# Kernel optimization log

Measured on AMD Instinct MI355X. Metric: run time of the kernel, lower is better.

The kernel has to match this reference:

```python
import jax, jax.numpy as jnp
import numpy as np

N = 10000        # num_nodes
E = 160000       # num_edges (before self loops)
D_IN = 256       # input_dim
H = 128          # hidden_dim (= per-head out_channels)
HEADS = 4
HD = HEADS * H   # 512
L = 16           # num_layers
OUT = 1024       # output_dim
G = 8            # num graphs in batch
EPS = 1e-5


def _layer_norm(x, w, b):
    m = jnp.mean(x, axis=-1, keepdims=True)
    v = jnp.mean(jnp.square(x - m), axis=-1, keepdims=True)
    return (x - m) / jnp.sqrt(v + EPS) * w + b


def setup_inputs() -> dict:
    key = jax.random.key(0)
    ks = jax.random.split(key, 20)
    s = 0.05
    x = jax.random.normal(ks[0], (N, D_IN), jnp.float32)
    edge_index = jax.random.randint(ks[1], (2, E), 0, N, dtype=jnp.int64)
    batch = jnp.sort(jax.random.randint(ks[2], (N,), 0, G, dtype=jnp.int64))
    return {
        "x": x,
        "edge_index": edge_index,
        "batch": batch,
        "W_in": jax.random.normal(ks[3], (D_IN, H), jnp.float32) * s,
        "b_in": jnp.zeros((H,), jnp.float32),
        "ln_in_w": jnp.ones((H,), jnp.float32),
        "ln_in_b": jnp.zeros((H,), jnp.float32),
        "Wsrc": jax.random.normal(ks[4], (L, H, HD), jnp.float32) * s,
        "Wdst": jax.random.normal(ks[5], (L, H, HD), jnp.float32) * s,
        "att_src": jax.random.normal(ks[6], (L, HEADS, H), jnp.float32) * s,
        "att_dst": jax.random.normal(ks[7], (L, HEADS, H), jnp.float32) * s,
        "Wout": jax.random.normal(ks[8], (L, HD, H), jnp.float32) * s,
        "bout": jnp.zeros((L, H), jnp.float32),
        "ln_w": jnp.ones((L, H), jnp.float32),
        "ln_b": jnp.zeros((L, H), jnp.float32),
        "Wp1": jax.random.normal(ks[9], (H, OUT), jnp.float32) * s,
        "bp1": jnp.zeros((OUT,), jnp.float32),
        "Wp2": jax.random.normal(ks[10], (OUT, OUT), jnp.float32) * s,
        "bp2": jnp.zeros((OUT,), jnp.float32),
    }


def reference(x, edge_index, batch, W_in, b_in, ln_in_w, ln_in_b,
              Wsrc, Wdst, att_src, att_dst, Wout, bout, ln_w, ln_b,
              Wp1, bp1, Wp2, bp2):
    # add self loops once (same edge set every layer)
    loop = jnp.arange(N, dtype=edge_index.dtype)
    e_src = jnp.concatenate([edge_index[0], loop])  # x_j (source)
    e_dst = jnp.concatenate([edge_index[1], loop])  # x_i (target / aggregate index)

    h = jax.nn.relu(_layer_norm(x @ W_in + b_in, ln_in_w, ln_in_b))  # [N, H]

    for l in range(L):
        hs = (h[e_src] @ Wsrc[l]).reshape(-1, HEADS, H)  # [E2, heads, H]
        hd = (h[e_dst] @ Wdst[l]).reshape(-1, HEADS, H)
        a = jnp.sum(hs * att_src[l], axis=-1) + jnp.sum(hd * att_dst[l], axis=-1)  # [E2, heads]
        a = jax.nn.leaky_relu(a, 0.2)
        # NOTE: faithful to source -- softmax over HEADS per edge, not over neighbors
        a = jax.nn.softmax(a, axis=-1)
        msg = (hs * a[..., None]).reshape(-1, HD)  # [E2, HD]
        agg = jax.ops.segment_sum(msg, e_dst, num_segments=N)  # [N, HD]
        out = agg @ Wout[l] + bout[l]
        h = jax.nn.relu(_layer_norm(out + h, ln_w[l], ln_b[l]))  # residual: H == H

    g = jax.ops.segment_max(h, batch, num_segments=G)  # global max pool [G, H]
    g = jax.nn.relu(g @ Wp1 + bp1)
    return g @ Wp2 + bp2  # [G, OUT]
```

## Files before the change

### kernel.cpp

```cpp
#include <hip/hip_runtime.h>
#include <hip/hip_bf16.h>

#define N_NODES 10000
#define E_EDGES 160000
#define E2 (E_EDGES + N_NODES)
#define D_IN 256
#define H 128
#define HEADS 4
#define HD 512
#define L_LAYERS 16
#define OUT_DIM 1024
#define G_GRAPHS 8
#define EPS 1e-5f
#define SPAD 10016

typedef unsigned short ushort_t;
typedef __attribute__((ext_vector_type(8))) short short8;
typedef __attribute__((ext_vector_type(4))) float f32x4;
typedef __attribute__((ext_vector_type(4))) unsigned u32x4;

__device__ __forceinline__ f32x4 mfma16(short8 a, short8 b, f32x4 c) {
    return __builtin_amdgcn_mfma_f32_16x16x32_bf16(a, b, c, 0, 0, 0);
}
__device__ __forceinline__ unsigned short f2b(float f) {
    unsigned u = __float_as_uint(f);
    u += 0x7fffu + ((u >> 16) & 1u);
    return (unsigned short)(u >> 16);
}
__device__ __forceinline__ float b2f(unsigned short b) {
    return __uint_as_float((unsigned)b << 16);
}
__device__ __forceinline__ unsigned pk2(float lo, float hi) {
    __hip_bfloat162 p = __float22bfloat162_rn(make_float2(lo, hi));
    return *(unsigned*)&p;
}

__global__ void k_zero(int* deg, int* cur, unsigned* g) {
    int i = blockIdx.x * blockDim.x + threadIdx.x;
    if (i < N_NODES) { deg[i] = 0; cur[i] = 0; }
    if (i < G_GRAPHS * H) g[i] = 0u;
}

__global__ void k_count(const int* ei, int* deg) {
    int e = blockIdx.x * blockDim.x + threadIdx.x;
    if (e >= E2) return;
    int d = (e < E_EDGES) ? ei[E_EDGES + e] : (e - E_EDGES);
    atomicAdd(&deg[d], 1);
}

__global__ void k_scan(const int* deg, int* rs) {
    __shared__ int s[1024];
    int t = threadIdx.x;
    int base = t * 10;
    int loc[10], run = 0;
    #pragma unroll
    for (int i = 0; i < 10; i++) {
        int idx = base + i;
        int v = (idx < N_NODES) ? deg[idx] : 0;
        loc[i] = run; run += v;
    }
    s[t] = run;
    __syncthreads();
    for (int off = 1; off < 1024; off <<= 1) {
        int xv = (t >= off) ? s[t - off] : 0;
        __syncthreads();
        s[t] += xv;
        __syncthreads();
    }
    int excl = s[t] - run;
    #pragma unroll
    for (int i = 0; i < 10; i++) {
        int idx = base + i;
        if (idx <= N_NODES) rs[idx] = excl + loc[i];
    }
}

__global__ void k_fill(const int* ei, const int* rs, int* cur, int* elist) {
    int e = blockIdx.x * blockDim.x + threadIdx.x;
    if (e >= E2) return;
    int s, d;
    if (e < E_EDGES) { s = ei[e]; d = ei[E_EDGES + e]; }
    else { s = d = e - E_EDGES; }
    int pos = atomicAdd(&cur[d], 1);
    elist[rs[d] + pos] = s;
}

__global__ __launch_bounds__(256) void k_vw(const float* __restrict__ Wsrc,
        const float* __restrict__ Wdst, const float* __restrict__ att_src,
        const float* __restrict__ att_dst, float* __restrict__ vsrc,
        float* __restrict__ vdst) {
    int t = threadIdx.x, w = t >> 6, lane = t & 63;
    int unit = blockIdx.x * 4 + w;
    int j = unit & 127, head = (unit >> 7) & 3, l = unit >> 9;
    int k2 = lane * 2;
    const float2 ws = *(const float2*)(Wsrc + (size_t)l * H * HD + (size_t)j * HD + head * 128 + k2);
    const float2 wd = *(const float2*)(Wdst + (size_t)l * H * HD + (size_t)j * HD + head * 128 + k2);
    const float2 as = *(const float2*)(att_src + (size_t)l * HEADS * H + head * 128 + k2);
    const float2 ad = *(const float2*)(att_dst + (size_t)l * HEADS * H + head * 128 + k2);
    float p = ws.x * as.x + ws.y * as.y;
    float q = wd.x * ad.x + wd.y * ad.y;
    #pragma unroll
    for (int off = 32; off > 0; off >>= 1) {
        p += __shfl_down(p, off);
        q += __shfl_down(q, off);
    }
    if (lane == 0) {
        vsrc[(size_t)l * HD + head * H + j] = p;
        vdst[(size_t)l * HD + head * H + j] = q;
    }
}

__global__ __launch_bounds__(256) void k_mm(const float* __restrict__ Wsrc,
        const float* __restrict__ Wout, float* __restrict__ M) {
    __shared__ float As[32][33];
    __shared__ float Bs[32][128];
    int bid = blockIdx.x;
    int q = bid & 3, hh = (bid >> 2) & 3, l = bid >> 4;
    int t = threadIdx.x;
    int ty = t >> 4, tx = t & 15;
    const float* WsB = Wsrc + (size_t)l * H * HD + (size_t)hh * 128;
    const float* WoB = Wout + (size_t)l * HD * H + (size_t)hh * 128 * H;
    float acc[2][8];
    #pragma unroll
    for (int r = 0; r < 2; r++)
        #pragma unroll
        for (int c = 0; c < 8; c++) acc[r][c] = 0.f;
    for (int kt = 0; kt < 4; kt++) {
        #pragma unroll
        for (int i = 0; i < 4; i++) {
            int lin = i * 256 + t;
            int rr = lin >> 5, cc = lin & 31;
            As[rr][cc] = WsB[(size_t)(q * 32 + rr) * HD + kt * 32 + cc];
        }
        #pragma unroll
        for (int i = 0; i < 16; i++) {
            int lin = i * 256 + t;
            int rr = lin >> 7, cc = lin & 127;
            Bs[rr][cc] = WoB[(size_t)(kt * 32 + rr) * H + cc];
        }
        __syncthreads();
        #pragma unroll
        for (int kk = 0; kk < 32; kk++) {
            float a0 = As[ty * 2][kk], a1 = As[ty * 2 + 1][kk];
            float4 b0 = *(const float4*)&Bs[kk][tx * 8];
            float4 b1 = *(const float4*)&Bs[kk][tx * 8 + 4];
            acc[0][0] += a0 * b0.x; acc[0][1] += a0 * b0.y;
            acc[0][2] += a0 * b0.z; acc[0][3] += a0 * b0.w;
            acc[0][4] += a0 * b1.x; acc[0][5] += a0 * b1.y;
            acc[0][6] += a0 * b1.z; acc[0][7] += a0 * b1.w;
            acc[1][0] += a1 * b0.x; acc[1][1] += a1 * b0.y;
            acc[1][2] += a1 * b0.z; acc[1][3] += a1 * b0.w;
            acc[1][4] += a1 * b1.x; acc[1][5] += a1 * b1.y;
            acc[1][6] += a1 * b1.z; acc[1][7] += a1 * b1.w;
        }
        __syncthreads();
    }
    #pragma unroll
    for (int r = 0; r < 2; r++)
        #pragma unroll
        for (int c = 0; c < 8; c++)
            M[(size_t)l * HD * H + (size_t)(hh * 128 + q * 32 + ty * 2 + r) * H + tx * 8 + c]
                = acc[r][c];
}

__global__ void k_pack_out2(const float* M, ushort_t* Wh, ushort_t* Wl) {
    int idx = blockIdx.x * 256 + threadIdx.x;
    int l = idx >> 16, rem = idx & 65535;
    int k = rem >> 7, col = rem & 127;
    float v = M[(size_t)l * HD * H + (size_t)k * H + col];
    unsigned short hi = f2b(v);
    unsigned short lo = f2b(v - b2f(hi));
    int nt = col >> 4, ks = k >> 5, lhi = (k >> 3) & 3, llo = col & 15, j = k & 7;
    size_t addr = (size_t)l * 65536 + (((size_t)(nt * 16 + ks) * 64) + lhi * 16 + llo) * 8 + j;
    Wh[addr] = hi;
    Wl[addr] = lo;
}

__global__ void k_pack_win(const float* W, ushort_t* Wp) {
    int idx = blockIdx.x * 256 + threadIdx.x;
    int k = idx >> 7, col = idx & 127;
    float v = W[(size_t)k * H + col];
    int nt = col >> 4, ks = k >> 5, lhi = (k >> 3) & 3, llo = col & 15, j = k & 7;
    Wp[(((size_t)(nt * 8 + ks) * 64) + lhi * 16 + llo) * 8 + j] = f2b(v);
}

__global__ __launch_bounds__(256) void k_in_mfma(
        const float* __restrict__ x, const ushort_t* __restrict__ WpI,
        const float* __restrict__ b_in, const float* __restrict__ lnw,
        const float* __restrict__ lnb, const float* __restrict__ vs,
        const float* __restrict__ vd, float* __restrict__ as0, float* __restrict__ ad0,
        float* __restrict__ h, ushort_t* __restrict__ hb) {
    __shared__ float part1[4][16], part2[4][16];
    __shared__ float apart[4][8][16];
    int t = threadIdx.x, w = t >> 6, lane = t & 63;
    int row0 = blockIdx.x * 16;
    int ar = lane & 15, ac = (lane >> 4) * 8;
    short8 a[8];
    #pragma unroll
    for (int ks = 0; ks < 8; ks++) {
        const float* xp = x + (size_t)(row0 + ar) * D_IN + ks * 32 + ac;
        float4 xa = *(const float4*)xp;
        float4 xb = *(const float4*)(xp + 4);
        u32x4 u;
        u.x = pk2(xa.x, xa.y); u.y = pk2(xa.z, xa.w);
        u.z = pk2(xb.x, xb.y); u.w = pk2(xb.z, xb.w);
        a[ks] = *(short8*)&u;
    }
    const ushort_t* B0 = WpI + ((size_t)(w * 2 + 0) * 8) * 64 * 8;
    const ushort_t* B1 = WpI + ((size_t)(w * 2 + 1) * 8) * 64 * 8;
    f32x4 c0 = {0.f, 0.f, 0.f, 0.f}, c1 = {0.f, 0.f, 0.f, 0.f};
    #pragma unroll
    for (int ks = 0; ks < 8; ks++) {
        short8 b0 = *(const short8*)(B0 + ((size_t)ks * 64 + lane) * 8);
        short8 b1 = *(const short8*)(B1 + ((size_t)ks * 64 + lane) * 8);
        c0 = mfma16(a[ks], b0, c0);
        c1 = mfma16(a[ks], b1, c1);
    }
    int col0 = w * 32 + ar, col1 = w * 32 + 16 + ar;
    int rb = (lane >> 4) * 4;
    float v0[4], v1[4], y0[4], y1[4];
    #pragma unroll
    for (int r = 0; r < 4; r++) {
        v0[r] = c0[r] + b_in[col0];
        v1[r] = c1[r] + b_in[col1];
        float p1 = v0[r] + v1[r];
        float p2 = v0[r] * v0[r] + v1[r] * v1[r];
        #pragma unroll
        for (int off = 1; off < 16; off <<= 1) {
            p1 += __shfl_xor(p1, off);
            p2 += __shfl_xor(p2, off);
        }
        if (ar == 0) { part1[w][rb + r] = p1; part2[w][rb + r] = p2; }
    }
    __syncthreads();
    #pragma unroll
    for (int r = 0; r < 4; r++) {
        int lr = rb + r;
        int row = row0 + lr;
        float s1 = part1[0][lr] + part1[1][lr] + part1[2][lr] + part1[3][lr];
        float s2 = part2[0][lr] + part2[1][lr] + part2[2][lr] + part2[3][lr];
        float m = s1 * (1.f / 128.f);
        float var = s2 * (1.f / 128.f) - m * m;
        float is = rsqrtf(var + EPS);
        y0[r] = fmaxf((v0[r] - m) * is * lnw[col0] + lnb[col0], 0.f);
        y1[r] = fmaxf((v1[r] - m) * is * lnw[col1] + lnb[col1], 0.f);
        h[(size_t)row * H + col0] = y0[r];
        h[(size_t)row * H + col1] = y1[r];
        hb[(size_t)row * H + col0] = f2b(y0[r]);
        hb[(size_t)row * H + col1] = f2b(y1[r]);
    }
    #pragma unroll
    for (int comp = 0; comp < 8; comp++) {
        float vc0 = (comp < 4) ? vs[comp * H + col0] : vd[(comp - 4) * H + col0];
        float vc1 = (comp < 4) ? vs[comp * H + col1] : vd[(comp - 4) * H + col1];
        float p[4];
        #pragma unroll
        for (int r = 0; r < 4; r++) p[r] = y0[r] * vc0 + y1[r] * vc1;
        #pragma unroll
        for (int off = 1; off < 16; off <<= 1)
            #pragma unroll
            for (int r = 0; r < 4; r++) p[r] += __shfl_xor(p[r], off);
        if (ar == 0)
            #pragma unroll
            for (int r = 0; r < 4; r++) apart[w][comp][rb + r] = p[r];
    }
    __syncthreads();
    if (t < 128) {
        int lr = t >> 3, comp = t & 7;
        float s = apart[0][comp][lr] + apart[1][comp][lr]
                + apart[2][comp][lr] + apart[3][comp][lr];
        int node = row0 + lr;
        if (comp < 4) as0[node * 4 + comp] = s;
        else          ad0[node * 4 + comp - 4] = s;
    }
}

#define ACC1(uv, wt) do { \
    acc[0] += (wt) * __uint_as_float((uv).x << 16); \
    acc[1] += (wt) * __uint_as_float((uv).x & 0xffff0000u); \
    acc[2] += (wt) * __uint_as_float((uv).y << 16); \
    acc[3] += (wt) * __uint_as_float((uv).y & 0xffff0000u); \
    acc[4] += (wt) * __uint_as_float((uv).z << 16); \
    acc[5] += (wt) * __uint_as_float((uv).z & 0xffff0000u); \
    acc[6] += (wt) * __uint_as_float((uv).w << 16); \
    acc[7] += (wt) * __uint_as_float((uv).w & 0xffff0000u); \
} while (0)

__global__ __launch_bounds__(512) void k_aggout(
        const ushort_t* __restrict__ hb, const float4* __restrict__ as4,
        const float4* __restrict__ ad4, const int* __restrict__ rs,
        const int* __restrict__ elist, const ushort_t* __restrict__ Wh,
        const ushort_t* __restrict__ Wl, const float* __restrict__ bout,
        const float* __restrict__ lnw, const float* __restrict__ lnb,
        const float* __restrict__ vsn, const float* __restrict__ vdn,
        float* __restrict__ asn, float* __restrict__ adn, int doAlpha,
        float* __restrict__ h, ushort_t* __restrict__ hbo, int l) {
    __shared__ ushort_t frag[16 * 64 * 8];
    __shared__ int sl[8][64];
    __shared__ float wl[8][64][4];
    __shared__ float part1[8][16], part2[8][16];
    __shared__ float apart[8][8][16];
    int t = threadIdx.x, w = t >> 6, lane = t & 63;
    int base = blockIdx.x * 16;
    int head = lane >> 4;
    int j8 = (lane & 15) * 8;

    for (int q = 0; q < 2; q++) {
        int r = w * 2 + q;
        int node = base + r;
        int start = rs[node], end = rs[node + 1];
        float4 adv = ad4[node];
        float acc[8];
        #pragma unroll
        for (int i = 0; i < 8; i++) acc[i] = 0.f;
        for (int c0 = start; c0 < end; c0 += 64) {
            int cnt = min(64, end - c0);
            if (lane < cnt) {
                int s = elist[c0 + lane];
                sl[w][lane] = s;
                float4 av = as4[s];
                float l0 = av.x + adv.x, l1 = av.y + adv.y, l2 = av.z + adv.z, l3 = av.w + adv.w;
                l0 = (l0 > 0.f) ? l0 : 0.2f * l0;
                l1 = (l1 > 0.f) ? l1 : 0.2f * l1;
                l2 = (l2 > 0.f) ? l2 : 0.2f * l2;
                l3 = (l3 > 0.f) ? l3 : 0.2f * l3;
                float mx = fmaxf(fmaxf(l0, l1), fmaxf(l2, l3));
                float e0 = expf(l0 - mx), e1 = expf(l1 - mx), e2 = expf(l2 - mx), e3 = expf(l3 - mx);
                float inv = 1.f / (e0 + e1 + e2 + e3);
                wl[w][lane][0] = e0 * inv;
                wl[w][lane][1] = e1 * inv;
                wl[w][lane][2] = e2 * inv;
                wl[w][lane][3] = e3 * inv;
            }
            __asm__ volatile("s_waitcnt lgkmcnt(0)" ::: "memory");
            int j = 0;
            if (cnt >= 4) {
                u32x4 b0, b1, b2, b3;
                float q0, q1, q2, q3;
                {
                    int s0 = sl[w][0], s1 = sl[w][1], s2 = sl[w][2], s3 = sl[w][3];
                    q0 = wl[w][0][head]; q1 = wl[w][1][head];
                    q2 = wl[w][2][head]; q3 = wl[w][3][head];
                    b0 = *(const u32x4*)(hb + (size_t)s0 * H + j8);
                    b1 = *(const u32x4*)(hb + (size_t)s1 * H + j8);
                    b2 = *(const u32x4*)(hb + (size_t)s2 * H + j8);
                    b3 = *(const u32x4*)(hb + (size_t)s3 * H + j8);
                }
                for (j = 4; j + 3 < cnt; j += 4) {
                    int s0 = sl[w][j], s1 = sl[w][j + 1], s2 = sl[w][j + 2], s3 = sl[w][j + 3];
                    u32x4 n0 = *(const u32x4*)(hb + (size_t)s0 * H + j8);
                    u32x4 n1 = *(const u32x4*)(hb + (size_t)s1 * H + j8);
                    u32x4 n2 = *(const u32x4*)(hb + (size_t)s2 * H + j8);
                    u32x4 n3 = *(const u32x4*)(hb + (size_t)s3 * H + j8);
                    float r0 = wl[w][j][head], r1 = wl[w][j + 1][head];
                    float r2 = wl[w][j + 2][head], r3 = wl[w][j + 3][head];
                    ACC1(b0, q0); ACC1(b1, q1); ACC1(b2, q2); ACC1(b3, q3);
                    b0 = n0; q0 = r0; b1 = n1; q1 = r1;
                    b2 = n2; q2 = r2; b3 = n3; q3 = r3;
                }
                ACC1(b0, q0); ACC1(b1, q1); ACC1(b2, q2); ACC1(b3, q3);
            }
            for (; j < cnt; j++) {
                int s = sl[w][j];
                float wt = wl[w][j][head];
                u32x4 uv = *(const u32x4*)(hb + (size_t)s * H + j8);
                ACC1(uv, wt);
            }
        }
        u32x4 o;
        o.x = pk2(acc[0], acc[1]);
        o.y = pk2(acc[2], acc[3]);
        o.z = pk2(acc[4], acc[5]);
        o.w = pk2(acc[6], acc[7]);
        int ksn = head * 4 + ((lane >> 2) & 3);
        int gidx = ((lane & 3) * 16 + r) * 16 + (ksn ^ r);
        *(u32x4*)((char*)frag + gidx * 16) = o;
    }
    __syncthreads();

    const ushort_t* WLh = Wh + (size_t)l * 65536;
    const ushort_t* WLl = Wl + (size_t)l * 65536;
    short8 a[16];
    #pragma unroll
    for (int ks = 0; ks < 16; ks++) {
        int gidx = lane * 16 + (ks ^ (lane & 15));
        a[ks] = *(const short8*)((const char*)frag + gidx * 16);
    }
    int ar = lane & 15;
    f32x4 c = {0.f, 0.f, 0.f, 0.f};
    #pragma unroll
    for (int ks = 0; ks < 16; ks++) {
        short8 bh = *(const short8*)(WLh + ((size_t)(w * 16 + ks) * 64 + lane) * 8);
        c = mfma16(a[ks], bh, c);
    }
    #pragma unroll
    for (int ks = 0; ks < 16; ks++) {
        short8 bl = *(const short8*)(WLl + ((size_t)(w * 16 + ks) * 64 + lane) * 8);
        c = mfma16(a[ks], bl, c);
    }

    const float* bo = bout + (size_t)l * H;
    const float* gw = lnw + (size_t)l * H;
    const float* gb = lnb + (size_t)l * H;
    int col = w * 16 + ar;
    int rb = (lane >> 4) * 4;
    float v[4], y[4];
    #pragma unroll
    for (int r = 0; r < 4; r++) {
        int row = base + rb + r;
        v[r] = c[r] + bo[col] + h[(size_t)row * H + col];
        float p1 = v[r];
        float p2 = v[r] * v[r];
        #pragma unroll
        for (int off = 1; off < 16; off <<= 1) {
            p1 += __shfl_xor(p1, off);
            p2 += __shfl_xor(p2, off);
        }
        if (ar == 0) { part1[w][rb + r] = p1; part2[w][rb + r] = p2; }
    }
    __syncthreads();
    #pragma unroll
    for (int r = 0; r < 4; r++) {
        int lr = rb + r;
        int row = base + lr;
        float s1 = 0.f, s2 = 0.f;
        #pragma unroll
        for (int ww = 0; ww < 8; ww++) { s1 += part1[ww][lr]; s2 += part2[ww][lr]; }
        float m = s1 * (1.f / 128.f);
        float var = s2 * (1.f / 128.f) - m * m;
        float is = rsqrtf(var + EPS);
        y[r] = fmaxf((v[r] - m) * is * gw[col] + gb[col], 0.f);
        h[(size_t)row * H + col] = y[r];
        hbo[(size_t)row * H + col] = f2b(y[r]);
    }

    if (doAlpha) {
        #pragma unroll
        for (int comp = 0; comp < 8; comp++) {
            float vc = (comp < 4) ? vsn[comp * H + col] : vdn[(comp - 4) * H + col];
            float p[4];
            #pragma unroll
            for (int r = 0; r < 4; r++) p[r] = y[r] * vc;
            #pragma unroll
            for (int off = 1; off < 16; off <<= 1)
                #pragma unroll
                for (int r = 0; r < 4; r++) p[r] += __shfl_xor(p[r], off);
            if (ar == 0)
                #pragma unroll
                for (int r = 0; r < 4; r++) apart[w][comp][rb + r] = p[r];
        }
        __syncthreads();
        if (t < 128) {
            int lr = t >> 3, comp = t & 7;
            float s = 0.f;
            #pragma unroll
            for (int ww = 0; ww < 8; ww++) s += apart[ww][comp][lr];
            int node = base + lr;
            if (comp < 4) asn[node * 4 + comp] = s;
            else          adn[node * 4 + comp - 4] = s;
        }
    }
}

__global__ void k_pool(const float* __restrict__ h, const int* __restrict__ batch,
                       unsigned* __restrict__ g) {
    __shared__ float lm[G_GRAPHS][H];
    int t = threadIdx.x;
    #pragma unroll
    for (int i = 0; i < G_GRAPHS; i++) lm[i][t] = 0.f;
    int n0 = blockIdx.x * 100, n1 = n0 + 100;
    for (int n = n0; n < n1; n++) {
        int b = batch[n];
        lm[b][t] = fmaxf(lm[b][t], h[(size_t)n * H + t]);
    }
    #pragma unroll
    for (int i = 0; i < G_GRAPHS; i++)
        atomicMax(&g[i * H + t], __float_as_uint(lm[i][t]));
}

__global__ void k_mlp1(const unsigned* __restrict__ g, const float* __restrict__ Wp1,
                       const float* __restrict__ bp1, float* __restrict__ g1) {
    __shared__ float gs[H];
    int gr = blockIdx.x >> 2, ch = blockIdx.x & 3;
    int t = threadIdx.x;
    if (t < H) gs[t] = __uint_as_float(g[gr * H + t]);
    __syncthreads();
    int col = ch * 256 + t;
    float acc = 0.f;
    for (int k = 0; k < H; k++) acc += gs[k] * Wp1[(size_t)k * OUT_DIM + col];
    acc += bp1[col];
    g1[(size_t)gr * OUT_DIM + col] = fmaxf(acc, 0.f);
}

__global__ void k_mlp2(const float* __restrict__ g1, const float* __restrict__ Wp2,
                       const float* __restrict__ bp2, float* __restrict__ out) {
    __shared__ float gs[OUT_DIM];
    __shared__ float part[4][64];
    int gr = blockIdx.x >> 4, ch = blockIdx.x & 15;
    int t = threadIdx.x;
    int ci = t & 63, si = t >> 6;
    for (int i = t; i < OUT_DIM; i += 256) gs[i] = g1[(size_t)gr * OUT_DIM + i];
    __syncthreads();
    int col = ch * 64 + ci;
    float acc = 0.f;
    for (int k = si * 256; k < si * 256 + 256; k++)
        acc += gs[k] * Wp2[(size_t)k * OUT_DIM + col];
    part[si][ci] = acc;
    __syncthreads();
    if (si == 0) {
        float r = part[0][ci] + part[1][ci] + part[2][ci] + part[3][ci] + bp2[col];
        out[(size_t)gr * OUT_DIM + col] = r;
    }
}

extern "C" void kernel_launch(void* const* d_in, const int* in_sizes, int n_in,
                              void* d_out, int out_size, void* d_ws, size_t ws_size,
                              hipStream_t stream) {
    const float* x       = (const float*)d_in[0];
    const int*   ei      = (const int*)d_in[1];
    const int*   batch   = (const int*)d_in[2];
    const float* W_in    = (const float*)d_in[3];
    const float* b_in    = (const float*)d_in[4];
    const float* ln_in_w = (const float*)d_in[5];
    const float* ln_in_b = (const float*)d_in[6];
    const float* Wsrc    = (const float*)d_in[7];
    const float* Wdst    = (const float*)d_in[8];
    const float* att_src = (const float*)d_in[9];
    const float* att_dst = (const float*)d_in[10];
    const float* Wout    = (const float*)d_in[11];
    const float* bout    = (const float*)d_in[12];
    const float* ln_w    = (const float*)d_in[13];
    const float* ln_b    = (const float*)d_in[14];
    const float* Wp1     = (const float*)d_in[15];
    const float* bp1     = (const float*)d_in[16];
    const float* Wp2     = (const float*)d_in[17];
    const float* bp2     = (const float*)d_in[18];

    char* w = (char*)d_ws;
    auto alloc = [&](size_t bytes) { void* p = w; w += (bytes + 255) & ~(size_t)255; return p; };
    float*     h     = (float*)alloc((size_t)N_NODES * H * 4);
    ushort_t*  hb0   = (ushort_t*)alloc((size_t)SPAD * H * 2);
    ushort_t*  hb1   = (ushort_t*)alloc((size_t)SPAD * H * 2);
    float*     as0   = (float*)alloc((size_t)SPAD * HEADS * 4);
    float*     ad0   = (float*)alloc((size_t)SPAD * HEADS * 4);
    float*     as1   = (float*)alloc((size_t)SPAD * HEADS * 4);
    float*     ad1   = (float*)alloc((size_t)SPAD * HEADS * 4);
    float*     vsrc  = (float*)alloc((size_t)L_LAYERS * HD * 4);
    float*     vdst  = (float*)alloc((size_t)L_LAYERS * HD * 4);
    float*     M     = (float*)alloc((size_t)L_LAYERS * HD * H * 4);
    ushort_t*  WpH   = (ushort_t*)alloc((size_t)L_LAYERS * 65536 * 2);
    ushort_t*  WpL   = (ushort_t*)alloc((size_t)L_LAYERS * 65536 * 2);
    ushort_t*  WpI   = (ushort_t*)alloc((size_t)D_IN * H * 2);
    int*       deg   = (int*)alloc((size_t)N_NODES * 4);
    int*       rs    = (int*)alloc((size_t)(N_NODES + 1) * 4);
    int*       cur   = (int*)alloc((size_t)N_NODES * 4);
    int*       elist = (int*)alloc((size_t)E2 * 4);
    unsigned*  g     = (unsigned*)alloc((size_t)G_GRAPHS * H * 4);
    float*     g1    = (float*)alloc((size_t)G_GRAPHS * OUT_DIM * 4);

    k_zero<<<40, 256, 0, stream>>>(deg, cur, g);
    k_count<<<(E2 + 255) / 256, 256, 0, stream>>>(ei, deg);
    k_scan<<<1, 1024, 0, stream>>>(deg, rs);
    k_fill<<<(E2 + 255) / 256, 256, 0, stream>>>(ei, rs, cur, elist);
    k_vw<<<2048, 256, 0, stream>>>(Wsrc, Wdst, att_src, att_dst, vsrc, vdst);
    k_mm<<<256, 256, 0, stream>>>(Wsrc, Wout, M);
    k_pack_out2<<<4096, 256, 0, stream>>>(M, WpH, WpL);
    k_pack_win<<<128, 256, 0, stream>>>(W_in, WpI);
    k_in_mfma<<<N_NODES / 16, 256, 0, stream>>>(x, WpI, b_in, ln_in_w, ln_in_b,
                                                vsrc, vdst, as0, ad0, h, hb0);

    for (int l = 0; l < L_LAYERS; l++) {
        const ushort_t* hbi = (l & 1) ? hb1 : hb0;
        ushort_t*       hbo = (l & 1) ? hb0 : hb1;
        const float* aA = (l & 1) ? as1 : as0;
        const float* dA = (l & 1) ? ad1 : ad0;
        float* aB = (l & 1) ? as0 : as1;
        float* dB = (l & 1) ? ad0 : ad1;
        int ln = (l + 1 < L_LAYERS) ? (l + 1) : (L_LAYERS - 1);
        k_aggout<<<N_NODES / 16, 512, 0, stream>>>(
            hbi, (const float4*)aA, (const float4*)dA, rs, elist, WpH, WpL,
            bout, ln_w, ln_b, vsrc + (size_t)ln * HD, vdst + (size_t)ln * HD,
            aB, dB, (l + 1 < L_LAYERS) ? 1 : 0, h, hbo, l);
    }

    k_pool<<<100, 128, 0, stream>>>(h, batch, g);
    k_mlp1<<<G_GRAPHS * 4, 256, 0, stream>>>(g, Wp1, bp1, g1);
    k_mlp2<<<G_GRAPHS * 16, 256, 0, stream>>>(g1, Wp2, bp2, (float*)d_out);
}
```

Before: 681.4 us.

## Reorder nodes by in-degree so aggregation blocks get balanced work

Adds a counting sort of nodes by in-degree (histogram, bin scan, scatter) that builds a permutation. The fused aggregate/output kernel now processes nodes in that order, so the 16 nodes in a block, and the two nodes each warp handles, have similar edge counts. This targets idle warps waiting on the highest-degree node in their block. In exchange, each block's rows are no longer contiguous, so row reads and writes of h and the attention scalars become scattered, and the one-time setup gains three small kernel launches.

```diff
diff --git a/kernel.cpp b/kernel.cpp
--- a/kernel.cpp
+++ b/kernel.cpp
@@ -35,10 +35,11 @@
     return *(unsigned*)&p;
 }
 
-__global__ void k_zero(int* deg, int* cur, unsigned* g) {
+__global__ void k_zero(int* deg, int* cur, unsigned* g, int* hist, int* cur2) {
     int i = blockIdx.x * blockDim.x + threadIdx.x;
     if (i < N_NODES) { deg[i] = 0; cur[i] = 0; }
     if (i < G_GRAPHS * H) g[i] = 0u;
+    if (i < 256) { hist[i] = 0; cur2[i] = 0; }
 }
 
 __global__ void k_count(const int* ei, int* deg) {
@@ -83,6 +84,36 @@
     else { s = d = e - E_EDGES; }
     int pos = atomicAdd(&cur[d], 1);
     elist[rs[d] + pos] = s;
+}
+
+__global__ void k_hist(const int* deg, int* hist) {
+    int i = blockIdx.x * blockDim.x + threadIdx.x;
+    if (i >= N_NODES) return;
+    int b = min(deg[i], 255);
+    atomicAdd(&hist[b], 1);
+}
+
+__global__ void k_binscan(const int* hist, int* binoff) {
+    __shared__ int s[256];
+    int t = threadIdx.x;
+    int v = hist[t];
+    s[t] = v;
+    __syncthreads();
+    for (int off = 1; off < 256; off <<= 1) {
+        int xv = (t >= off) ? s[t - off] : 0;
+        __syncthreads();
+        s[t] += xv;
+        __syncthreads();
+    }
+    binoff[t] = s[t] - v;
+}
+
+__global__ void k_scatter(const int* deg, const int* binoff, int* cur2, int* perm) {
+    int i = blockIdx.x * blockDim.x + threadIdx.x;
+    if (i >= N_NODES) return;
+    int b = min(deg[i], 255);
+    int pos = atomicAdd(&cur2[b], 1);
+    perm[binoff[b] + pos] = i;
 }
 
 __global__ __launch_bounds__(256) void k_vw(const float* __restrict__ Wsrc,
@@ -289,12 +320,13 @@
 __global__ __launch_bounds__(512) void k_aggout(
         const ushort_t* __restrict__ hb, const float4* __restrict__ as4,
         const float4* __restrict__ ad4, const int* __restrict__ rs,
-        const int* __restrict__ elist, const ushort_t* __restrict__ Wh,
-        const ushort_t* __restrict__ Wl, const float* __restrict__ bout,
-        const float* __restrict__ lnw, const float* __restrict__ lnb,
-        const float* __restrict__ vsn, const float* __restrict__ vdn,
-        float* __restrict__ asn, float* __restrict__ adn, int doAlpha,
-        float* __restrict__ h, ushort_t* __restrict__ hbo, int l) {
+        const int* __restrict__ elist, const int* __restrict__ perm,
+        const ushort_t* __restrict__ Wh, const ushort_t* __restrict__ Wl,
+        const float* __restrict__ bout, const float* __restrict__ lnw,
+        const float* __restrict__ lnb, const float* __restrict__ vsn,
+        const float* __restrict__ vdn, float* __restrict__ asn,
+        float* __restrict__ adn, int doAlpha, float* __restrict__ h,
+        ushort_t* __restrict__ hbo, int l) {
     __shared__ ushort_t frag[16 * 64 * 8];
     __shared__ int sl[8][64];
     __shared__ float wl[8][64][4];
@@ -307,7 +339,7 @@
 
     for (int q = 0; q < 2; q++) {
         int r = w * 2 + q;
-        int node = base + r;
+        int node = perm[base + r];
         int start = rs[node], end = rs[node + 1];
         float4 adv = ad4[node];
         float acc[8];
@@ -405,10 +437,11 @@
     int col = w * 16 + ar;
     int rb = (lane >> 4) * 4;
     float v[4], y[4];
+    int rowg[4];
     #pragma unroll
     for (int r = 0; r < 4; r++) {
-        int row = base + rb + r;
-        v[r] = c[r] + bo[col] + h[(size_t)row * H + col];
+        rowg[r] = perm[base + rb + r];
+        v[r] = c[r] + bo[col] + h[(size_t)rowg[r] * H + col];
         float p1 = v[r];
         float p2 = v[r] * v[r];
         #pragma unroll
@@ -422,7 +455,7 @@
     #pragma unroll
     for (int r = 0; r < 4; r++) {
         int lr = rb + r;
-        int row = base + lr;
+        int row = rowg[r];
         float s1 = 0.f, s2 = 0.f;
         #pragma unroll
         for (int ww = 0; ww < 8; ww++) { s1 += part1[ww][lr]; s2 += part2[ww][lr]; }
@@ -455,7 +488,7 @@
             float s = 0.f;
             #pragma unroll
             for (int ww = 0; ww < 8; ww++) s += apart[ww][comp][lr];
-            int node = base + lr;
+            int node = perm[base + lr];
             if (comp < 4) asn[node * 4 + comp] = s;
             else          adn[node * 4 + comp - 4] = s;
         }
@@ -555,13 +588,20 @@
     int*       rs    = (int*)alloc((size_t)(N_NODES + 1) * 4);
     int*       cur   = (int*)alloc((size_t)N_NODES * 4);
     int*       elist = (int*)alloc((size_t)E2 * 4);
+    int*       perm  = (int*)alloc((size_t)N_NODES * 4);
+    int*       hist  = (int*)alloc(256 * 4);
+    int*       binoff= (int*)alloc(256 * 4);
+    int*       cur2  = (int*)alloc(256 * 4);
     unsigned*  g     = (unsigned*)alloc((size_t)G_GRAPHS * H * 4);
     float*     g1    = (float*)alloc((size_t)G_GRAPHS * OUT_DIM * 4);
 
-    k_zero<<<40, 256, 0, stream>>>(deg, cur, g);
+    k_zero<<<40, 256, 0, stream>>>(deg, cur, g, hist, cur2);
     k_count<<<(E2 + 255) / 256, 256, 0, stream>>>(ei, deg);
     k_scan<<<1, 1024, 0, stream>>>(deg, rs);
     k_fill<<<(E2 + 255) / 256, 256, 0, stream>>>(ei, rs, cur, elist);
+    k_hist<<<40, 256, 0, stream>>>(deg, hist);
+    k_binscan<<<1, 256, 0, stream>>>(hist, binoff);
+    k_scatter<<<40, 256, 0, stream>>>(deg, binoff, cur2, perm);
     k_vw<<<2048, 256, 0, stream>>>(Wsrc, Wdst, att_src, att_dst, vsrc, vdst);
     k_mm<<<256, 256, 0, stream>>>(Wsrc, Wout, M);
     k_pack_out2<<<4096, 256, 0, stream>>>(M, WpH, WpL);
@@ -578,7 +618,7 @@
         float* dB = (l & 1) ? ad0 : ad1;
         int ln = (l + 1 < L_LAYERS) ? (l + 1) : (L_LAYERS - 1);
         k_aggout<<<N_NODES / 16, 512, 0, stream>>>(
-            hbi, (const float4*)aA, (const float4*)dA, rs, elist, WpH, WpL,
+            hbi, (const float4*)aA, (const float4*)dA, rs, elist, perm, WpH, WpL,
             bout, ln_w, ln_b, vsrc + (size_t)ln * HD, vdst + (size_t)ln * HD,
             aB, dB, (l + 1 < L_LAYERS) ? 1 : 0, h, hbo, l);
     }
```

Measured after the change: 797.5 us. 1.17x slower.
